# Kernel optimization log

Measured on AMD Instinct MI355X. Metric: run time of the kernel, lower is better.

Reference implementation:

```python
import jax, jax.numpy as jnp
import numpy as np

K = 25          # kernel_size (number of B-spline control points)
DEGREE = 1      # open linear B-spline -> 2 nonzero basis weights per edge
N_NODES = 200000
N_EDGES = 6400000


def setup_inputs() -> dict:
    key = jax.random.key(0)
    k1, k2, k3, k4 = jax.random.split(key, 4)
    x = jax.random.normal(k1, (N_NODES, 2), dtype=jnp.float32)
    weight = jax.random.normal(k2, (K, 2, 1), dtype=jnp.float32)
    edges = jax.random.randint(k3, (2, N_EDGES), 0, N_NODES, dtype=jnp.int64)
    pseudo = jax.random.uniform(k4, (N_EDGES, 1), dtype=jnp.float32)
    return {"x": x, "weight": weight, "edges": edges, "pseudo": pseudo}


def reference(x, weight, edges, pseudo):
    # spline_conv with norm=True, no root_weight, no bias (forward only passes
    # x, edges, pseudo, weight, kernel_size=[25], is_open_spline=[1], degree, norm).
    row, col = edges[0], edges[1]   # messages gathered from col, scattered to row
    n = x.shape[0]

    # --- B-spline basis (open, degree 1, 1-D pseudo) ---
    p = pseudo[:, 0]                      # [E]
    v = p * (K - DEGREE)                  # [E], in [0, K-1)
    lo = jnp.floor(v)
    frac = v - lo                         # [E]
    i0 = jnp.clip(lo.astype(jnp.int32), 0, K - 1)       # [E]
    i1 = jnp.clip(i0 + 1, 0, K - 1)                     # [E]

    # --- gather + weighting: msg_e = sum_s basis[e,s] * x[col_e] @ W[idx[e,s]] ---
    xj = x[col]                                         # [E, 2]
    m0 = jnp.einsum('ef,efo->eo', xj, weight[i0])       # [E, 1]
    m1 = jnp.einsum('ef,efo->eo', xj, weight[i1])       # [E, 1]
    msg = (1.0 - frac)[:, None] * m0 + frac[:, None] * m1   # [E, 1]

    # --- scatter-add to target nodes ---
    out = jax.ops.segment_sum(msg, row, num_segments=n)     # [N, 1]

    # --- degree normalization (norm=True) ---
    deg = jax.ops.segment_sum(jnp.ones_like(p), row, num_segments=n)  # [N]
    out = out / jnp.clip(deg, 1.0, None)[:, None]
    return out
```

## Files before the change

### kernel.cpp

```cpp
#include <hip/hip_runtime.h>

#define KK 25
#define FP_SCALE 268435456.0f
#define FP_INV   (1.0f / 268435456.0f)

#define TPB 256
#define EPT 16
#define EPB (TPB * EPT)
#define WSHIFT 10
#define WNODE 1024
#define MAXBINS 256
#define CAP 36864

typedef unsigned long long u64;

__global__ void zero_counts(unsigned* __restrict__ p, int n) {
    int i = blockIdx.x * blockDim.x + threadIdx.x;
    if (i < n) p[i] = 0u;
}

__global__ __launch_bounds__(TPB, 6) void phase1(
    const float* __restrict__ x,
    const float* __restrict__ w,
    const int* __restrict__ row,
    const int* __restrict__ col,
    const float* __restrict__ pseudo,
    unsigned* __restrict__ bucket,
    unsigned* __restrict__ gcount,
    int n_edges)
{
    __shared__ float4  wq[32];
    __shared__ unsigned bin_cnt[MAXBINS];
    __shared__ unsigned bin_start[MAXBINS];
    __shared__ unsigned joff[MAXBINS];
    __shared__ unsigned wtot[4];
    __shared__ unsigned stage[EPB];
    __shared__ unsigned char bin_map[EPB];

    const int tid = threadIdx.x;
    if (tid < KK) {
        int i1 = min(tid + 1, KK - 1);
        wq[tid] = make_float4(w[2 * tid], w[2 * tid + 1],
                              w[2 * i1],  w[2 * i1 + 1]);
    }
    bin_cnt[tid] = 0u;
    __syncthreads();

    const long long base = (long long)blockIdx.x * EPB;
    const bool full = (base + EPB) <= (long long)n_edges;
    const int nloc = full ? EPB
                          : (int)(((long long)n_edges - base) > 0
                                      ? ((long long)n_edges - base) : 0LL);

    unsigned pk[EPT];
    if (full) {
        const int4* r4 = (const int4*)&row[base + (long long)tid * EPT];
        int rloc[EPT];
        #pragma unroll
        for (int q = 0; q < EPT / 4; ++q) {
            int4 rr = r4[q];
            rloc[4 * q + 0] = rr.x; rloc[4 * q + 1] = rr.y;
            rloc[4 * q + 2] = rr.z; rloc[4 * q + 3] = rr.w;
        }
        #pragma unroll
        for (int k = 0; k < EPT; ++k) {
            int r = rloc[k];
            int bin = r >> WSHIFT;
            unsigned rank = atomicAdd(&bin_cnt[bin], 1u);
            pk[k] = ((unsigned)bin << 22) | (rank << 10)
                  | (unsigned)(r & (WNODE - 1));
        }
    } else {
        for (int k = 0; k < EPT; ++k) {
            int i = tid * EPT + k;
            if (i < nloc) {
                int r = row[base + i];
                int bin = r >> WSHIFT;
                unsigned rank = atomicAdd(&bin_cnt[bin], 1u);
                pk[k] = ((unsigned)bin << 22) | (rank << 10)
                      | (unsigned)(r & (WNODE - 1));
            } else pk[k] = 0xFFFFFFFFu;
        }
    }
    __syncthreads();

    {
        unsigned v = bin_cnt[tid];
        unsigned incl = v;
        #pragma unroll
        for (int d = 1; d < 64; d <<= 1) {
            unsigned t = __shfl_up(incl, d, 64);
            if ((tid & 63) >= d) incl += t;
        }
        if ((tid & 63) == 63) wtot[tid >> 6] = incl;
        __syncthreads();
        unsigned off = 0;
        const int wv = tid >> 6;
        #pragma unroll
        for (int ww = 0; ww < 4; ++ww)
            if (ww < wv) off += wtot[ww];
        unsigned st = off + incl - v;
        bin_start[tid] = st;
        unsigned gb = v ? atomicAdd(&gcount[tid], v) : 0u;
        joff[tid] = gb - st;
    }
    __syncthreads();

    const float2* __restrict__ x2 = (const float2*)x;
    if (full) {
        const int4*   c4 = (const int4*)&col[base + (long long)tid * EPT];
        const float4* p4 = (const float4*)&pseudo[base + (long long)tid * EPT];
        #pragma unroll
        for (int q = 0; q < EPT / 4; ++q) {
            int4   cc = c4[q];
            float4 pp = p4[q];
            int   ca[4] = {cc.x, cc.y, cc.z, cc.w};
            float pa[4] = {pp.x, pp.y, pp.z, pp.w};
            #pragma unroll
            for (int j = 0; j < 4; ++j) {
                unsigned p = pk[4 * q + j];
                float vv = pa[j] * (float)(KK - 1);
                int   i0 = (int)vv;
                float fr = vv - (float)i0;
                float4 qw = wq[i0];
                float2 xj = x2[ca[j]];
                float wa = qw.x + fr * (qw.z - qw.x);
                float wb = qw.y + fr * (qw.w - qw.y);
                float msg = xj.x * wa + xj.y * wb;
                unsigned ub = (__float_as_uint(msg) + 0x200u) & 0xFFFFFC00u;
                unsigned entry = ub | (p & (WNODE - 1));
                unsigned bin = p >> 22;
                unsigned pos = bin_start[bin] + ((p >> 10) & 0xFFFu);
                stage[pos] = entry;
                bin_map[pos] = (unsigned char)bin;
            }
        }
    } else {
        for (int k = 0; k < EPT; ++k) {
            int i = tid * EPT + k;
            if (i < nloc) {
                unsigned p = pk[k];
                long long e = base + i;
                int c = col[e];
                float ps = pseudo[e];
                float vv = ps * (float)(KK - 1);
                int   i0 = (int)vv;
                float fr = vv - (float)i0;
                float4 qw = wq[i0];
                float2 xj = x2[c];
                float wa = qw.x + fr * (qw.z - qw.x);
                float wb = qw.y + fr * (qw.w - qw.y);
                float msg = xj.x * wa + xj.y * wb;
                unsigned ub = (__float_as_uint(msg) + 0x200u) & 0xFFFFFC00u;
                unsigned entry = ub | (p & (WNODE - 1));
                unsigned bin = p >> 22;
                unsigned pos = bin_start[bin] + ((p >> 10) & 0xFFFu);
                stage[pos] = entry;
                bin_map[pos] = (unsigned char)bin;
            }
        }
    }
    __syncthreads();

    for (int i = tid; i < nloc; i += TPB) {
        unsigned entry = stage[i];
        unsigned b = bin_map[i];
        unsigned g = joff[b] + (unsigned)i;
        if (g < CAP) bucket[(size_t)b * CAP + g] = entry;
    }
}

__global__ __launch_bounds__(1024) void phase2(
    const unsigned* __restrict__ bucket,
    const unsigned* __restrict__ gcount,
    float* __restrict__ out, int n_nodes)
{
    __shared__ u64 acc[WNODE];
    const int tid = threadIdx.x;
    const int bin = blockIdx.x;

    acc[tid] = 0ULL;
    __syncthreads();

    unsigned cnt = gcount[bin];
    if (cnt > CAP) cnt = CAP;
    const unsigned* __restrict__ bb = bucket + (size_t)bin * CAP;

    const unsigned nvec = cnt >> 2;
    const uint4* __restrict__ b4 = (const uint4*)bb;
    for (unsigned i = tid; i < nvec; i += 1024) {
        uint4 e4 = b4[i];
        unsigned ee[4] = {e4.x, e4.y, e4.z, e4.w};
        #pragma unroll
        for (int j = 0; j < 4; ++j) {
            unsigned e = ee[j];
            float msg = __uint_as_float(e & 0xFFFFFC00u);
            long long fx = (long long)llrintf(msg * FP_SCALE);
            atomicAdd(&acc[e & (WNODE - 1)], ((u64)fx << 16) | 1ULL);
        }
    }
    for (unsigned i = (nvec << 2) + tid; i < cnt; i += 1024) {
        unsigned e = bb[i];
        float msg = __uint_as_float(e & 0xFFFFFC00u);
        long long fx = (long long)llrintf(msg * FP_SCALE);
        atomicAdd(&acc[e & (WNODE - 1)], ((u64)fx << 16) | 1ULL);
    }
    __syncthreads();

    const int node = (bin << WSHIFT) + tid;
    if (node < n_nodes) {
        u64 t = acc[tid];
        int count = (int)(t & 0xFFFFULL);
        long long sf = ((long long)t) >> 16;
        float sum = (float)sf * FP_INV;
        out[node] = sum / (float)max(count, 1);
    }
}

__global__ void zero_acc(u64* __restrict__ p, int n) {
    int i = blockIdx.x * blockDim.x + threadIdx.x;
    if (i < n) p[i] = 0ULL;
}

__global__ void edge_kernel_flat(const float* __restrict__ x,
                                 const float* __restrict__ w,
                                 const int* __restrict__ row,
                                 const int* __restrict__ col,
                                 const float* __restrict__ pseudo,
                                 u64* __restrict__ acc,
                                 int n_edges) {
    __shared__ float wsm[KK * 2];
    if (threadIdx.x < KK * 2) wsm[threadIdx.x] = w[threadIdx.x];
    __syncthreads();

    const float2* __restrict__ x2 = (const float2*)x;
    int e = blockIdx.x * blockDim.x + threadIdx.x;
    if (e >= n_edges) return;

    int r = row[e];
    int c = col[e];
    float p = pseudo[e];
    float vv = p * (float)(KK - 1);
    float lo = floorf(vv);
    float fr = vv - lo;
    int i0 = min(max((int)lo, 0), KK - 1);
    int i1 = min(i0 + 1, KK - 1);
    float2 xj = x2[c];
    float m0 = xj.x * wsm[2 * i0] + xj.y * wsm[2 * i0 + 1];
    float m1 = xj.x * wsm[2 * i1] + xj.y * wsm[2 * i1 + 1];
    float msg = (1.0f - fr) * m0 + fr * m1;

    long long fx = (long long)llrintf(msg * FP_SCALE);
    atomicAdd(&acc[r], ((u64)fx << 16) + 1ULL);
}

__global__ void finalize_flat(const u64* __restrict__ acc,
                              float* __restrict__ out, int n) {
    int i = blockIdx.x * blockDim.x + threadIdx.x;
    if (i >= n) return;
    u64 t = acc[i];
    int count = (int)(t & 0xFFFFULL);
    long long sf = ((long long)t) >> 16;
    float sum = (float)sf * FP_INV;
    out[i] = sum / (float)max(count, 1);
}

extern "C" void kernel_launch(void* const* d_in, const int* in_sizes, int n_in,
                              void* d_out, int out_size, void* d_ws, size_t ws_size,
                              hipStream_t stream) {
    const float* x      = (const float*)d_in[0];
    const float* w      = (const float*)d_in[1];
    const int*   edges  = (const int*)d_in[2];
    const float* pseudo = (const float*)d_in[3];

    const int n_edges = in_sizes[3];
    const int n_nodes = out_size;

    const int* row = edges;
    const int* col = edges + n_edges;

    const int nbins = (n_nodes + WNODE - 1) >> WSHIFT;
    const size_t need = 4096 + (size_t)nbins * CAP * sizeof(unsigned);

    if (nbins <= MAXBINS && ws_size >= need) {
        unsigned* gcount = (unsigned*)d_ws;
        unsigned* bucket = (unsigned*)((char*)d_ws + 4096);

        zero_counts<<<1, MAXBINS, 0, stream>>>(gcount, MAXBINS);

        int blocks = (n_edges + EPB - 1) / EPB;
        phase1<<<blocks, TPB, 0, stream>>>(x, w, row, col, pseudo,
                                           bucket, gcount, n_edges);

        phase2<<<nbins, 1024, 0, stream>>>(bucket, gcount,
                                           (float*)d_out, n_nodes);
    } else {
        u64* acc = (u64*)d_ws;
        zero_acc<<<(n_nodes + 255) / 256, 256, 0, stream>>>(acc, n_nodes);
        int blocks = (n_edges + 255) / 256;
        edge_kernel_flat<<<blocks, 256, 0, stream>>>(x, w, row, col, pseudo,
                                                     acc, n_edges);
        finalize_flat<<<(n_nodes + 255) / 256, 256, 0, stream>>>(acc,
                                                                 (float*)d_out,
                                                                 n_nodes);
    }
}
```

Before: 172.1 us.

## Split global bin counters into 8 sub-buckets and batch x gathers

Each destination bin's global counter and bucket are split into 8 sub-buckets chosen by block index, which spreads the global atomicAdd contention from phase1 blocks across 8 counters. Phase2 then walks all 8 sub-buckets for its bin. Phase1 also issues 8 x-gathers up front per half-iteration to raise memory-level parallelism. The cost is more phase2 loop overhead, partially filled sub-buckets, and a per-sub capacity that could overflow if edges are skewed.

```diff
diff --git a/kernel.cpp b/kernel.cpp
--- a/kernel.cpp
+++ b/kernel.cpp
@@ -10,7 +10,8 @@
 #define WSHIFT 10
 #define WNODE 1024
 #define MAXBINS 256
-#define CAP 36864
+#define NSUB 8
+#define SUBCAP 4736
 
 typedef unsigned long long u64;
 
@@ -32,12 +33,13 @@
     __shared__ float4  wq[32];
     __shared__ unsigned bin_cnt[MAXBINS];
     __shared__ unsigned bin_start[MAXBINS];
-    __shared__ unsigned joff[MAXBINS];
+    __shared__ unsigned gbase[MAXBINS];
     __shared__ unsigned wtot[4];
     __shared__ unsigned stage[EPB];
     __shared__ unsigned char bin_map[EPB];
 
     const int tid = threadIdx.x;
+    const unsigned sub = (unsigned)(blockIdx.x & (NSUB - 1));
     if (tid < KK) {
         int i1 = min(tid + 1, KK - 1);
         wq[tid] = make_float4(w[2 * tid], w[2 * tid + 1],
@@ -99,10 +101,8 @@
         #pragma unroll
         for (int ww = 0; ww < 4; ++ww)
             if (ww < wv) off += wtot[ww];
-        unsigned st = off + incl - v;
-        bin_start[tid] = st;
-        unsigned gb = v ? atomicAdd(&gcount[tid], v) : 0u;
-        joff[tid] = gb - st;
+        bin_start[tid] = off + incl - v;
+        gbase[tid] = v ? atomicAdd(&gcount[(tid << 3) | sub], v) : 0u;
     }
     __syncthreads();
 
@@ -111,27 +111,30 @@
         const int4*   c4 = (const int4*)&col[base + (long long)tid * EPT];
         const float4* p4 = (const float4*)&pseudo[base + (long long)tid * EPT];
         #pragma unroll
-        for (int q = 0; q < EPT / 4; ++q) {
-            int4   cc = c4[q];
-            float4 pp = p4[q];
-            int   ca[4] = {cc.x, cc.y, cc.z, cc.w};
-            float pa[4] = {pp.x, pp.y, pp.z, pp.w};
+        for (int h = 0; h < 2; ++h) {
+            int4   cc0 = c4[2 * h], cc1 = c4[2 * h + 1];
+            float4 pp0 = p4[2 * h], pp1 = p4[2 * h + 1];
+            float2 xj[8];
+            xj[0] = x2[cc0.x]; xj[1] = x2[cc0.y];
+            xj[2] = x2[cc0.z]; xj[3] = x2[cc0.w];
+            xj[4] = x2[cc1.x]; xj[5] = x2[cc1.y];
+            xj[6] = x2[cc1.z]; xj[7] = x2[cc1.w];
+            float pa[8] = {pp0.x, pp0.y, pp0.z, pp0.w,
+                           pp1.x, pp1.y, pp1.z, pp1.w};
             #pragma unroll
-            for (int j = 0; j < 4; ++j) {
-                unsigned p = pk[4 * q + j];
+            for (int j = 0; j < 8; ++j) {
+                unsigned p = pk[8 * h + j];
                 float vv = pa[j] * (float)(KK - 1);
                 int   i0 = (int)vv;
                 float fr = vv - (float)i0;
                 float4 qw = wq[i0];
-                float2 xj = x2[ca[j]];
                 float wa = qw.x + fr * (qw.z - qw.x);
                 float wb = qw.y + fr * (qw.w - qw.y);
-                float msg = xj.x * wa + xj.y * wb;
+                float msg = xj[j].x * wa + xj[j].y * wb;
                 unsigned ub = (__float_as_uint(msg) + 0x200u) & 0xFFFFFC00u;
-                unsigned entry = ub | (p & (WNODE - 1));
                 unsigned bin = p >> 22;
                 unsigned pos = bin_start[bin] + ((p >> 10) & 0xFFFu);
-                stage[pos] = entry;
+                stage[pos] = ub | (p & (WNODE - 1));
                 bin_map[pos] = (unsigned char)bin;
             }
         }
@@ -152,10 +155,9 @@
                 float wb = qw.y + fr * (qw.w - qw.y);
                 float msg = xj.x * wa + xj.y * wb;
                 unsigned ub = (__float_as_uint(msg) + 0x200u) & 0xFFFFFC00u;
-                unsigned entry = ub | (p & (WNODE - 1));
                 unsigned bin = p >> 22;
                 unsigned pos = bin_start[bin] + ((p >> 10) & 0xFFFu);
-                stage[pos] = entry;
+                stage[pos] = ub | (p & (WNODE - 1));
                 bin_map[pos] = (unsigned char)bin;
             }
         }
@@ -165,8 +167,9 @@
     for (int i = tid; i < nloc; i += TPB) {
         unsigned entry = stage[i];
         unsigned b = bin_map[i];
-        unsigned g = joff[b] + (unsigned)i;
-        if (g < CAP) bucket[(size_t)b * CAP + g] = entry;
+        unsigned idx = gbase[b] + ((unsigned)i - bin_start[b]);
+        if (idx < SUBCAP)
+            bucket[(size_t)((b << 3) | sub) * SUBCAP + idx] = entry;
     }
 }
 
@@ -182,28 +185,32 @@
     acc[tid] = 0ULL;
     __syncthreads();
 
-    unsigned cnt = gcount[bin];
-    if (cnt > CAP) cnt = CAP;
-    const unsigned* __restrict__ bb = bucket + (size_t)bin * CAP;
-
-    const unsigned nvec = cnt >> 2;
-    const uint4* __restrict__ b4 = (const uint4*)bb;
-    for (unsigned i = tid; i < nvec; i += 1024) {
-        uint4 e4 = b4[i];
-        unsigned ee[4] = {e4.x, e4.y, e4.z, e4.w};
-        #pragma unroll
-        for (int j = 0; j < 4; ++j) {
-            unsigned e = ee[j];
+    #pragma unroll
+    for (int sub = 0; sub < NSUB; ++sub) {
+        unsigned cnt = gcount[(bin << 3) | sub];
+        if (cnt > SUBCAP) cnt = SUBCAP;
+        const unsigned* __restrict__ bb =
+            bucket + (size_t)((bin << 3) | sub) * SUBCAP;
+
+        const unsigned nvec = cnt >> 2;
+        const uint4* __restrict__ b4 = (const uint4*)bb;
+        for (unsigned i = tid; i < nvec; i += 1024) {
+            uint4 e4 = b4[i];
+            unsigned ee[4] = {e4.x, e4.y, e4.z, e4.w};
+            #pragma unroll
+            for (int j = 0; j < 4; ++j) {
+                unsigned e = ee[j];
+                float msg = __uint_as_float(e & 0xFFFFFC00u);
+                long long fx = (long long)llrintf(msg * FP_SCALE);
+                atomicAdd(&acc[e & (WNODE - 1)], ((u64)fx << 16) | 1ULL);
+            }
+        }
+        for (unsigned i = (nvec << 2) + tid; i < cnt; i += 1024) {
+            unsigned e = bb[i];
             float msg = __uint_as_float(e & 0xFFFFFC00u);
             long long fx = (long long)llrintf(msg * FP_SCALE);
             atomicAdd(&acc[e & (WNODE - 1)], ((u64)fx << 16) | 1ULL);
         }
-    }
-    for (unsigned i = (nvec << 2) + tid; i < cnt; i += 1024) {
-        unsigned e = bb[i];
-        float msg = __uint_as_float(e & 0xFFFFFC00u);
-        long long fx = (long long)llrintf(msg * FP_SCALE);
-        atomicAdd(&acc[e & (WNODE - 1)], ((u64)fx << 16) | 1ULL);
     }
     __syncthreads();
 
@@ -280,13 +287,15 @@
     const int* col = edges + n_edges;
 
     const int nbins = (n_nodes + WNODE - 1) >> WSHIFT;
-    const size_t need = 4096 + (size_t)nbins * CAP * sizeof(unsigned);
+    const size_t need = 8192 +
+        (size_t)nbins * NSUB * SUBCAP * sizeof(unsigned);
 
     if (nbins <= MAXBINS && ws_size >= need) {
         unsigned* gcount = (unsigned*)d_ws;
-        unsigned* bucket = (unsigned*)((char*)d_ws + 4096);
-
-        zero_counts<<<1, MAXBINS, 0, stream>>>(gcount, MAXBINS);
+        unsigned* bucket = (unsigned*)((char*)d_ws + 8192);
+
+        zero_counts<<<(MAXBINS * NSUB + 255) / 256, 256, 0, stream>>>(
+            gcount, MAXBINS * NSUB);
 
         int blocks = (n_edges + EPB - 1) / EPB;
         phase1<<<blocks, TPB, 0, stream>>>(x, w, row, col, pseudo,
```

After: 177.6 us. 1.03x slower.
